# Optimization experiments

Hardware: AMD Instinct MI355X
Metric: run time of the kernel (lower is better)

Reference implementation:

```python
import jax, jax.numpy as jnp
import numpy as np

N = 131072
BETA = 1.0
E = float(np.e)
BISECT_ITERS = 60  # (v-u)/2^60 << 1e-5 threshold of FIND_MIN


def _smooth_l1(x, beta=BETA):
    d = jnp.abs(x)
    return jnp.where(d < beta, 0.5 * d * d / beta, d - 0.5 * beta)


def _safe_log(w):
    return jnp.log(jnp.maximum(w, 1e-12))


def _eps(w, wp, wh, beta=BETA):
    # epsilon(omega) = smooth_l1((omega-omega_hat)/2) + smooth_l1(log omega - log omega_p)
    return _smooth_l1((w - wh) * 0.5, beta) + _smooth_l1(_safe_log(w) - _safe_log(wp), beta)


def _eps_prime(w, wp, wh, beta=BETA):
    x = (w - wh) * 0.5
    diff = _safe_log(w) - _safe_log(wp)
    return 0.5 * jnp.clip(x / beta, -1.0, 1.0) + jnp.clip(diff / beta, -1.0, 1.0) / jnp.maximum(w, 1e-12)


def _sigma(w, wp, wh, beta=BETA):
    return w * _eps_prime(w, wp, wh, beta)


def _find_min(u, v, f):
    # Vectorized FIND_MIN bisection: fixed-trip bisection + boundary cases.
    u0, v0 = u, v

    def body(_, uv):
        uu, vv = uv
        m = (uu + vv) * 0.5
        c = f(m) >= 0
        return (jnp.where(c, uu, m), jnp.where(c, m, vv))

    uf, vf = jax.lax.fori_loop(0, BISECT_ITERS, body, (u, v))
    m = (uf + vf) * 0.5
    return jnp.where(f(u0) >= 0, u0, jnp.where(f(v0) <= 0, v0, m))


def _solve_o1(wp, wh, a1, b1, beta=BETA):
    w0 = b1 - a1
    fm_e = lambda u, v: _find_min(u, v, lambda w: _eps_prime(w, wp, wh, beta))
    fm_s = lambda u, v: _find_min(u, v, lambda w: _sigma(w, wp, wh, beta))
    branchA = jnp.maximum(w0, wh) < wp
    branchB = jnp.maximum(w0, wp) < wh
    cA = fm_e(jnp.maximum(w0, wh), wp)
    ebeta = float(np.exp(beta))
    # J1..J5 intervals from J_getter
    c2 = fm_e(jnp.maximum(w0, wp), jnp.minimum(float(np.exp(min(beta, 1.0))) * wp, wh))
    c3 = fm_e(jnp.maximum(jnp.maximum(w0, 2.0 * float(np.sqrt(beta))), jnp.maximum(wh - 2.0 * beta, ebeta * wp)), wh)
    base = jnp.maximum(w0, jnp.maximum(wh - 2.0 * beta, E * wp))
    c4 = fm_s(base, jnp.minimum(ebeta, wh))
    disc = jnp.sqrt(jnp.maximum(1.0 - 32.0 / jnp.maximum(wh * wh, 1e-12), 0.0))
    c5 = fm_s(base, jnp.minimum(jnp.minimum(ebeta * wp, wh), wh * 0.25 * (1.0 + disc)))
    c6 = fm_s(jnp.maximum(base, wh * 0.25 * (1.0 - disc)), jnp.minimum(ebeta * wp, wh))
    small = wh <= 4.0 * float(np.sqrt(2.0))
    cands = jnp.stack([w0, wh, c2, c3, c4, c5, c6], axis=-1)  # [N,7]
    evals = _eps(cands, wp[..., None], wh[..., None], beta)
    zeros = jnp.zeros_like(small)
    invalid = jnp.stack([zeros, zeros, zeros, zeros, ~small, small, small], axis=-1)
    evals = jnp.where(invalid, jnp.float32(1e30), evals)
    idx = jnp.argmin(evals, axis=-1)
    wB = jnp.take_along_axis(cands, idx[..., None], axis=-1)[..., 0]
    return jnp.where(branchA, cA, jnp.where(branchB, wB, w0))


def _solve_o2(dp, wp, a2, b2, beta=BETA):
    wh1 = 2.0 * (dp - a2)
    wh2 = 2.0 * (b2 - dp)
    trivial = wp >= jnp.maximum(wh1, wh2)
    w1 = _solve_o1(wp, wh1, a2, b2, beta)
    w2 = _solve_o1(wp, wh2, a2, b2, beta)
    pick1 = _eps(w1, wp, wh1, beta) <= _eps(w2, wp, wh2, beta)
    d = jnp.where(pick1, a2 + 0.5 * w1, b2 + 0.5 * w2)
    w = jnp.where(pick1, w1, w2)
    return jnp.where(trivial, dp, d), jnp.where(trivial, wp, w)


def _case_axis(pred, prop, cases, target, crop, axis):
    if axis == 0:
        lt, rb = cases[:, 0], cases[:, 1]
        d_id, o_id = 0, 2
    else:
        lt, rb = cases[:, 2], cases[:, 3]
        d_id, o_id = 1, 3
    pd, po = pred[:, d_id], pred[:, o_id]
    td, to = target[:, d_id], target[:, o_id]
    ca = 0.5 * (prop[:, d_id] + prop[:, o_id])
    da = prop[:, o_id] - prop[:, d_id]
    # right/bottom cut
    a1r = td - 0.5 * to
    b1r = (crop[:, axis] - ca) / da
    wr = _solve_o1(po, 2.0 * (pd - a1r), a1r, b1r)
    dr = a1r + 0.5 * wr
    # left/top cut
    a1l = -ca / da
    b1l = td + 0.5 * to
    wl = _solve_o1(po, 2.0 * (b1l - pd), a1l, b1l)
    dl = b1l - 0.5 * wl
    # both cut (source passes omega_p=pred[:,d_id] and crop[:,d_id] -- replicated)
    b2 = (crop[:, d_id] - ca) / da
    db, wb = _solve_o2(pd, pd, a1l, b2)
    none_c = (~lt) & (~rb)
    r_c = (~lt) & rb
    l_c = lt & (~rb)
    d_lab = jnp.where(none_c, td, jnp.where(r_c, dr, jnp.where(l_c, dl, db)))
    w_lab = jnp.where(none_c, to, jnp.where(r_c, wr, jnp.where(l_c, wl, wb)))
    return d_lab, w_lab


def setup_inputs() -> dict:
    key = jax.random.key(0)
    k = jax.random.split(key, 8)
    img = jax.random.normal(k[0], (1, 3, 128, 128), jnp.float32)
    pred = jax.random.normal(k[1], (N, 4), jnp.float32) * 0.3
    target = jax.random.normal(k[2], (N, 4), jnp.float32) * 0.3
    xy1 = jax.random.uniform(k[3], (N, 2), jnp.float32) * 800.0
    wh = jax.random.uniform(k[4], (N, 2), jnp.float32) * 180.0 + 20.0
    proposal_list = jnp.stack([xy1[:, 0], xy1[:, 1], xy1[:, 0] + wh[:, 0], xy1[:, 1] + wh[:, 1]], axis=1)
    crop_shapes = jax.random.uniform(k[5], (N, 4), jnp.float32) * 200.0 + 900.0
    cases = jax.random.bernoulli(k[6], 0.5, (N, 4))
    return {"img": img, "pred": pred, "target": target, "crop_shapes": crop_shapes,
            "proposal_list": proposal_list, "cases": cases, "sampling_results": 0}


def reference(img, pred, target, crop_shapes, proposal_list, cases, sampling_results):
    # target/pred dw,dh (cols 2,3) are exponentiated to widths/heights, as in forward
    predw = pred.at[:, 2:4].set(jnp.exp(pred[:, 2:4]))
    targw = target.at[:, 2:4].set(jnp.exp(target[:, 2:4]))
    d0, w0 = _case_axis(predw, proposal_list, cases, targw, crop_shapes, 0)
    d1, w1 = _case_axis(predw, proposal_list, cases, targw, crop_shapes, 1)
    # label layout [dx, dy, w, h] matching label[0..3] of the source
    return jnp.stack([d0, d1, w0, w1], axis=-1)
```

## Files before the change

kernel.cpp:

```cpp
#include <hip/hip_runtime.h>
#include <math.h>

#define BISECT_ITERS 60
#define N_ROWS 131072
#define N_PAIRS (2 * N_ROWS)
#define BLOCK 512
#define NW (BLOCK / 64)

#define E_CONST 2.71828182845904523536f
#define SMALL_THRESH 5.65685424949238019520f
#define LN2F 0.69314718055994530942f

__device__ __forceinline__ float log_cr(float wc) {
    double d = (double)wc;
    long long b = __double_as_longlong(d);
    int e = (int)((b >> 52) & 0x7FF) - 1023;
    double m = __longlong_as_double((b & 0x000FFFFFFFFFFFFFLL) |
                                    0x3FF0000000000000LL);
    if (m > 1.3333333333333333) {
        m *= 0.5;
        e += 1;
    }
    double s = (m - 1.0) / (m + 1.0);
    double s2 = s * s;
    double p = 1.0 / 17.0;
    p = fma(p, s2, 1.0 / 15.0);
    p = fma(p, s2, 1.0 / 13.0);
    p = fma(p, s2, 1.0 / 11.0);
    p = fma(p, s2, 1.0 / 9.0);
    p = fma(p, s2, 1.0 / 7.0);
    p = fma(p, s2, 1.0 / 5.0);
    p = fma(p, s2, 1.0 / 3.0);
    p = fma(p, s2, 1.0);
    double res = fma(2.0 * s, p, (double)e * 0.69314718055994530941723212145818);
    return (float)res;
}

__device__ __forceinline__ float safe_log_f(float w) {
    return log_cr(fmaxf(w, 1e-12f));
}

__device__ __forceinline__ float clip1f(float x) {
#pragma clang fp contract(off)
    return fminf(fmaxf(x, -1.0f), 1.0f);
}

__device__ __forceinline__ float sl1(float x) {
#pragma clang fp contract(off)
    float d = fabsf(x);
    return (d < 1.0f) ? (0.5f * d) * d : d - 0.5f;
}

__device__ __forceinline__ float eps_f(float w, float wh, float lwp) {
#pragma clang fp contract(off)
    return sl1((w - wh) * 0.5f) + sl1(safe_log_f(w) - lwp);
}

__device__ __forceinline__ float eps_prime_cr(float w, float wh, float lwp) {
#pragma clang fp contract(off)
    float x = (w - wh) * 0.5f;
    float diff = safe_log_f(w) - lwp;
    return 0.5f * clip1f(x) + clip1f(diff) / fmaxf(w, 1e-12f);
}

__device__ __forceinline__ float sigma_cr(float w, float wh, float lwp) {
#pragma clang fp contract(off)
    return w * eps_prime_cr(w, wh, lwp);
}

__device__ __forceinline__ float epsp_sign(float m, float wh, float lwp) {
    float wm = fmaxf(m, 1e-12f);
    float x = (m - wh) * 0.5f;
    float diff = __builtin_fmaf(LN2F, __builtin_amdgcn_logf(wm), -lwp);
    return __builtin_fmaf(0.5f * clip1f(x), wm, clip1f(diff));
}

__device__ float find_min_e(float u, float v, float wh, float lwp) {
#pragma clang fp contract(off)
    float u0 = u, v0 = v;
#pragma unroll 1
    for (int i = 0; i < BISECT_ITERS; ++i) {
        float m = (u + v) * 0.5f;
        bool frozen = (m == u) || (m == v);
        bool c = epsp_sign(m, wh, lwp) >= 0.0f;
        u = c ? u : m;
        v = c ? m : v;
        if (__all(frozen)) break;
    }
    float m = (u + v) * 0.5f;
    float r = m;
    if (eps_prime_cr(v0, wh, lwp) <= 0.0f) r = v0;
    if (eps_prime_cr(u0, wh, lwp) >= 0.0f) r = u0;
    return r;
}

struct PairP {
    float pd, po, td, to, a1r, b1r, a1l, b1l;
    int lt, rb;
};

__device__ __forceinline__ PairP load_pair(const float* __restrict__ pred,
                                           const float* __restrict__ target,
                                           const float* __restrict__ crop,
                                           const float* __restrict__ prop,
                                           const int* __restrict__ cases,
                                           int pair) {
#pragma clang fp contract(off)
    int row = pair >> 1, axis = pair & 1;
    int d_id = axis, o_id = axis + 2, r4 = row * 4;
    PairP P;
    P.pd = pred[r4 + d_id];
    P.po = (float)exp((double)pred[r4 + o_id]);
    P.td = target[r4 + d_id];
    P.to = (float)exp((double)target[r4 + o_id]);
    float p_d = prop[r4 + d_id];
    float p_o = prop[r4 + o_id];
    float ca = 0.5f * (p_d + p_o);
    float da = p_o - p_d;
    float crop_a = crop[r4 + axis];
    P.a1r = P.td - 0.5f * P.to;
    P.b1r = (crop_a - ca) / da;
    P.a1l = (-ca) / da;
    P.b1l = P.td + 0.5f * P.to;
    P.lt = cases[r4 + 2 * axis];
    P.rb = cases[r4 + 2 * axis + 1];
    return P;
}

__device__ float solve_B_large(float wp, float wh, float w0, float lwp) {
#pragma clang fp contract(off)
    float ewp = E_CONST * wp;
    float base = fmaxf(w0, fmaxf(wh - 2.0f, ewp));
    float disc = sqrtf(fmaxf(1.0f - 32.0f / fmaxf(wh * wh, 1e-12f), 0.0f));

    float u2 = fmaxf(w0, wp), v2 = fminf(ewp, wh);
    float u3 = fmaxf(fmaxf(w0, 2.0f), fmaxf(wh - 2.0f, ewp)), v3 = wh;
    float u5 = base, v5 = fminf(fminf(ewp, wh), (wh * 0.25f) * (1.0f + disc));
    float u6 = fmaxf(base, (wh * 0.25f) * (1.0f - disc)), v6 = fminf(ewp, wh);
    float u02 = u2, v02 = v2, u03 = u3, v03 = v3;
    float u05 = u5, v05 = v5, u06 = u6, v06 = v6;

#pragma unroll 1
    for (int i = 0; i < BISECT_ITERS; ++i) {
        float m2 = (u2 + v2) * 0.5f;
        float m3 = (u3 + v3) * 0.5f;
        float m5 = (u5 + v5) * 0.5f;
        float m6 = (u6 + v6) * 0.5f;
        bool fr = (m2 == u2 || m2 == v2) && (m3 == u3 || m3 == v3) &&
                  (m5 == u5 || m5 == v5) && (m6 == u6 || m6 == v6);
        bool c2 = epsp_sign(m2, wh, lwp) >= 0.0f;
        bool c3 = epsp_sign(m3, wh, lwp) >= 0.0f;
        bool c5 = (m5 * epsp_sign(m5, wh, lwp)) >= 0.0f;
        bool c6 = (m6 * epsp_sign(m6, wh, lwp)) >= 0.0f;
        u2 = c2 ? u2 : m2; v2 = c2 ? m2 : v2;
        u3 = c3 ? u3 : m3; v3 = c3 ? m3 : v3;
        u5 = c5 ? u5 : m5; v5 = c5 ? m5 : v5;
        u6 = c6 ? u6 : m6; v6 = c6 ? m6 : v6;
        if (__all(fr)) break;
    }

    float c2r = (u2 + v2) * 0.5f;
    if (eps_prime_cr(v02, wh, lwp) <= 0.0f) c2r = v02;
    if (eps_prime_cr(u02, wh, lwp) >= 0.0f) c2r = u02;
    float c3r = (u3 + v3) * 0.5f;
    if (eps_prime_cr(v03, wh, lwp) <= 0.0f) c3r = v03;
    if (eps_prime_cr(u03, wh, lwp) >= 0.0f) c3r = u03;
    float c5r = (u5 + v5) * 0.5f;
    if (sigma_cr(v05, wh, lwp) <= 0.0f) c5r = v05;
    if (sigma_cr(u05, wh, lwp) >= 0.0f) c5r = u05;
    float c6r = (u6 + v6) * 0.5f;
    if (sigma_cr(v06, wh, lwp) <= 0.0f) c6r = v06;
    if (sigma_cr(u06, wh, lwp) >= 0.0f) c6r = u06;

    float cands[7] = {w0, wh, c2r, c3r, 0.0f, c5r, c6r};
    float evals[7];
    evals[0] = eps_f(w0, wh, lwp);
    evals[1] = eps_f(wh, wh, lwp);
    evals[2] = eps_f(c2r, wh, lwp);
    evals[3] = eps_f(c3r, wh, lwp);
    evals[4] = 1e30f;
    evals[5] = eps_f(c5r, wh, lwp);
    evals[6] = eps_f(c6r, wh, lwp);

    float bestv = evals[0];
    float wB = cands[0];
#pragma unroll
    for (int j = 1; j < 7; ++j) {
        if (evals[j] < bestv) {
            bestv = evals[j];
            wB = cands[j];
        }
    }
    return wB;
}

__device__ float solve_B_small(float wp, float wh, float w0, float lwp) {
#pragma clang fp contract(off)
    float ewp = E_CONST * wp;
    float base = fmaxf(w0, fmaxf(wh - 2.0f, ewp));

    float u2 = fmaxf(w0, wp), v2 = fminf(ewp, wh);
    float u3 = fmaxf(fmaxf(w0, 2.0f), fmaxf(wh - 2.0f, ewp)), v3 = wh;
    float u4 = base, v4 = fminf(E_CONST, wh);
    float u02 = u2, v02 = v2, u03 = u3, v03 = v3, u04 = u4, v04 = v4;

#pragma unroll 1
    for (int i = 0; i < BISECT_ITERS; ++i) {
        float m2 = (u2 + v2) * 0.5f;
        float m3 = (u3 + v3) * 0.5f;
        float m4 = (u4 + v4) * 0.5f;
        bool fr = (m2 == u2 || m2 == v2) && (m3 == u3 || m3 == v3) &&
                  (m4 == u4 || m4 == v4);
        bool c2 = epsp_sign(m2, wh, lwp) >= 0.0f;
        bool c3 = epsp_sign(m3, wh, lwp) >= 0.0f;
        bool c4 = (m4 * epsp_sign(m4, wh, lwp)) >= 0.0f;
        u2 = c2 ? u2 : m2; v2 = c2 ? m2 : v2;
        u3 = c3 ? u3 : m3; v3 = c3 ? m3 : v3;
        u4 = c4 ? u4 : m4; v4 = c4 ? m4 : v4;
        if (__all(fr)) break;
    }

    float c2r = (u2 + v2) * 0.5f;
    if (eps_prime_cr(v02, wh, lwp) <= 0.0f) c2r = v02;
    if (eps_prime_cr(u02, wh, lwp) >= 0.0f) c2r = u02;
    float c3r = (u3 + v3) * 0.5f;
    if (eps_prime_cr(v03, wh, lwp) <= 0.0f) c3r = v03;
    if (eps_prime_cr(u03, wh, lwp) >= 0.0f) c3r = u03;
    float c4r = (u4 + v4) * 0.5f;
    if (sigma_cr(v04, wh, lwp) <= 0.0f) c4r = v04;
    if (sigma_cr(u04, wh, lwp) >= 0.0f) c4r = u04;

    float cands[7] = {w0, wh, c2r, c3r, c4r, 0.0f, 0.0f};
    float evals[7];
    evals[0] = eps_f(w0, wh, lwp);
    evals[1] = eps_f(wh, wh, lwp);
    evals[2] = eps_f(c2r, wh, lwp);
    evals[3] = eps_f(c3r, wh, lwp);
    evals[4] = eps_f(c4r, wh, lwp);
    evals[5] = 1e30f;
    evals[6] = 1e30f;

    float bestv = evals[0];
    float wB = cands[0];
#pragma unroll
    for (int j = 1; j < 7; ++j) {
        if (evals[j] < bestv) {
            bestv = evals[j];
            wB = cands[j];
        }
    }
    return wB;
}

__global__ __launch_bounds__(BLOCK)
void cabb_fused_kernel(const float* __restrict__ pred,
                       const float* __restrict__ target,
                       const float* __restrict__ crop,
                       const float* __restrict__ prop,
                       const int* __restrict__ cases,
                       float* __restrict__ out) {
#pragma clang fp contract(off)
    __shared__ float qb_wp[2 * BLOCK], qb_wh[2 * BLOCK], qb_w0[2 * BLOCK];
    __shared__ unsigned short qb_code[2 * BLOCK];
    __shared__ float qa_wp[BLOCK], qa_wh[BLOCK], qa_w0[BLOCK];
    __shared__ unsigned short qa_code[BLOCK];
    __shared__ float s_res[2 * BLOCK];
    __shared__ int s_cnt[NW][3];
    __shared__ int s_tot[3];

    int tid = threadIdx.x;
    int wid = tid >> 6;
    int lane = tid & 63;
    unsigned long long lower = (1ULL << lane) - 1ULL;
    int pair = blockIdx.x * BLOCK + tid;

    if (tid < 3) s_tot[tid] = 0;

    PairP P = load_pair(pred, target, crop, prop, cases, pair);

    bool need_b = P.lt && P.rb;
    bool need_l = P.lt && !P.rb;
    bool need_r = !P.lt && P.rb;

    int it_type[2] = {-1, -1};
    float it_wp[2], it_wh[2], it_w0[2];
    unsigned short it_code[2];
    int nit = 0;

    if (need_r || need_l) {
        float wp = P.po;
        float wh = need_l ? 2.0f * (P.b1l - P.pd) : 2.0f * (P.pd - P.a1r);
        float w0 = need_l ? (P.b1l - P.a1l) : (P.b1r - P.a1r);
        bool bA = fmaxf(w0, wh) < wp;
        bool bB = fmaxf(w0, wp) < wh;
        if (bA || bB) {
            it_type[0] = bA ? 2 : (wh <= SMALL_THRESH ? 1 : 0);
            it_wp[0] = wp; it_wh[0] = wh; it_w0[0] = w0;
            it_code[0] = (unsigned short)(tid * 2);
            nit = 1;
        }
    } else if (need_b) {
        float wh1 = 2.0f * (P.pd - P.a1l);
        float wh2 = 2.0f * (P.b1r - P.pd);
        bool trivial = P.pd >= fmaxf(wh1, wh2);
        if (!trivial) {
            float w0 = P.b1r - P.a1l;
            for (int s = 0; s < 2; ++s) {
                float wh = s ? wh2 : wh1;
                bool bA = fmaxf(w0, wh) < P.pd;
                bool bB = fmaxf(w0, P.pd) < wh;
                if (bA || bB) {
                    it_type[nit] = bA ? 2 : (wh <= SMALL_THRESH ? 1 : 0);
                    it_wp[nit] = P.pd; it_wh[nit] = wh; it_w0[nit] = w0;
                    it_code[nit] = (unsigned short)(tid * 2 + s);
                    ++nit;
                }
            }
        }
    }

    for (int k = 0; k < 2; ++k) {
        bool is0 = it_type[k] == 0, is1 = it_type[k] == 1, is2 = it_type[k] == 2;
        unsigned long long m0 = __ballot(is0);
        unsigned long long m1 = __ballot(is1);
        unsigned long long m2 = __ballot(is2);
        if (lane == 0) {
            s_cnt[wid][0] = __popcll(m0);
            s_cnt[wid][1] = __popcll(m1);
            s_cnt[wid][2] = __popcll(m2);
        }
        __syncthreads();
        if (it_type[k] >= 0) {
            int t = it_type[k];
            int base = s_tot[t];
            for (int w = 0; w < wid; ++w) base += s_cnt[w][t];
            unsigned long long mm = t == 0 ? m0 : (t == 1 ? m1 : m2);
            int pos = base + __popcll(mm & lower);
            if (t == 0) {
                qb_wp[pos] = it_wp[k]; qb_wh[pos] = it_wh[k];
                qb_w0[pos] = it_w0[k]; qb_code[pos] = it_code[k];
            } else if (t == 1) {
                int p2 = (2 * BLOCK - 1) - pos;
                qb_wp[p2] = it_wp[k]; qb_wh[p2] = it_wh[k];
                qb_w0[p2] = it_w0[k]; qb_code[p2] = it_code[k];
            } else {
                qa_wp[pos] = it_wp[k]; qa_wh[pos] = it_wh[k];
                qa_w0[pos] = it_w0[k]; qa_code[pos] = it_code[k];
            }
        }
        __syncthreads();
        if (tid < 3) {
            int s = 0;
            for (int w = 0; w < NW; ++w) s += s_cnt[w][tid];
            s_tot[tid] += s;
        }
        __syncthreads();
    }

    int nBl = s_tot[0], nBs = s_tot[1], nA = s_tot[2];

    for (int base = wid * 64; base < nBl; base += BLOCK) {
        int i = base + lane;
        if (i < nBl) {
            float wp = qb_wp[i], wh = qb_wh[i], w0 = qb_w0[i];
            float lwp = safe_log_f(wp);
            s_res[qb_code[i]] = solve_B_large(wp, wh, w0, lwp);
        }
    }
    for (int base = wid * 64; base < nBs; base += BLOCK) {
        int i = base + lane;
        if (i < nBs) {
            int idx = (2 * BLOCK - 1) - i;
            float wp = qb_wp[idx], wh = qb_wh[idx], w0 = qb_w0[idx];
            float lwp = safe_log_f(wp);
            s_res[qb_code[idx]] = solve_B_small(wp, wh, w0, lwp);
        }
    }
    for (int base = wid * 64; base < nA; base += BLOCK) {
        int i = base + lane;
        if (i < nA) {
            float wp = qa_wp[i], wh = qa_wh[i], w0 = qa_w0[i];
            float lwp = safe_log_f(wp);
            s_res[qa_code[i]] = find_min_e(fmaxf(w0, wh), wp, wh, lwp);
        }
    }
    __syncthreads();

    int row = pair >> 1, axis = pair & 1;
    int r4 = row * 4;
    float d_lab, w_lab;
    if (need_b) {
        float wh1 = 2.0f * (P.pd - P.a1l);
        float wh2 = 2.0f * (P.b1r - P.pd);
        bool trivial = P.pd >= fmaxf(wh1, wh2);
        if (trivial) {
            d_lab = P.pd;
            w_lab = P.pd;
        } else {
            float w0 = P.b1r - P.a1l;
            bool q1 = (fmaxf(w0, wh1) < P.pd) || (fmaxf(w0, P.pd) < wh1);
            bool q2 = (fmaxf(w0, wh2) < P.pd) || (fmaxf(w0, P.pd) < wh2);
            float s1 = q1 ? s_res[tid * 2] : w0;
            float s2 = q2 ? s_res[tid * 2 + 1] : w0;
            float lwp = safe_log_f(P.pd);
            bool pick1 = eps_f(s1, wh1, lwp) <= eps_f(s2, wh2, lwp);
            d_lab = pick1 ? (P.a1l + 0.5f * s1) : (P.b1r + 0.5f * s2);
            w_lab = pick1 ? s1 : s2;
        }
    } else if (need_l) {
        float wh = 2.0f * (P.b1l - P.pd);
        float w0 = P.b1l - P.a1l;
        bool q = (fmaxf(w0, wh) < P.po) || (fmaxf(w0, P.po) < wh);
        float s = q ? s_res[tid * 2] : w0;
        d_lab = P.b1l - 0.5f * s;
        w_lab = s;
    } else if (need_r) {
        float wh = 2.0f * (P.pd - P.a1r);
        float w0 = P.b1r - P.a1r;
        bool q = (fmaxf(w0, wh) < P.po) || (fmaxf(w0, P.po) < wh);
        float s = q ? s_res[tid * 2] : w0;
        d_lab = P.a1r + 0.5f * s;
        w_lab = s;
    } else {
        d_lab = P.td;
        w_lab = P.to;
    }

    out[r4 + axis] = d_lab;
    out[r4 + 2 + axis] = w_lab;
}

extern "C" void kernel_launch(void* const* d_in, const int* in_sizes, int n_in,
                              void* d_out, int out_size, void* d_ws, size_t ws_size,
                              hipStream_t stream) {
    const float* pred = (const float*)d_in[1];
    const float* target = (const float*)d_in[2];
    const float* crop = (const float*)d_in[3];
    const float* prop = (const float*)d_in[4];
    const int* cases = (const int*)d_in[5];
    float* out = (float*)d_out;

    cabb_fused_kernel<<<N_PAIRS / BLOCK, BLOCK, 0, stream>>>(
        pred, target, crop, prop, cases, out);
}
```

Measured before the change: 93.93 us.

## Use fast log filters with exact fallback for boundary checks and candidate selection

Endpoint sign checks, candidate-energy evaluation and the two-sided pick now use the hardware log2 approximation first. They fall back to the double-precision log only when the result lies within a tolerance band where the sign or ordering is ambiguous, which removes most of the expensive software log evaluations. The three per-queue solve loops are merged into one chunk loop that hands 64-lane chunks to wavefronts round-robin, so work is balanced across queues. The risk is that the tolerance thresholds might miss a case where the fast path disagrees with the exact path, and the fallback branches add divergence.

```diff
diff --git a/kernel.cpp b/kernel.cpp
--- a/kernel.cpp
+++ b/kernel.cpp
@@ -10,6 +10,7 @@
 #define E_CONST 2.71828182845904523536f
 #define SMALL_THRESH 5.65685424949238019520f
 #define LN2F 0.69314718055994530942f
+#define LOG1EM12 -27.63102111592854820f
 
 __device__ __forceinline__ float log_cr(float wc) {
     double d = (double)wc;
@@ -37,7 +38,8 @@
 }
 
 __device__ __forceinline__ float safe_log_f(float w) {
-    return log_cr(fmaxf(w, 1e-12f));
+    if (w <= 1e-12f) return LOG1EM12;
+    return log_cr(w);
 }
 
 __device__ __forceinline__ float clip1f(float x) {
@@ -66,6 +68,10 @@
 __device__ __forceinline__ float sigma_cr(float w, float wh, float lwp) {
 #pragma clang fp contract(off)
     return w * eps_prime_cr(w, wh, lwp);
+}
+
+__device__ __forceinline__ float nlogf(float w) {
+    return LN2F * __builtin_amdgcn_logf(fmaxf(w, 1e-12f));
 }
 
 __device__ __forceinline__ float epsp_sign(float m, float wh, float lwp) {
@@ -73,6 +79,30 @@
     float x = (m - wh) * 0.5f;
     float diff = __builtin_fmaf(LN2F, __builtin_amdgcn_logf(wm), -lwp);
     return __builtin_fmaf(0.5f * clip1f(x), wm, clip1f(diff));
+}
+
+__device__ __forceinline__ int fast_epsp_sgn(float x, float wh, float lwp) {
+    float wm = fmaxf(x, 1e-12f);
+    float F = epsp_sign(x, wh, lwp);
+    float tau = 2e-5f * (wm + 1.0f);
+    if (F > tau) return 1;
+    if (F < -tau) return -1;
+    return 0;
+}
+
+__device__ __forceinline__ int fast_sigma_sgn(float x, float wh, float lwp) {
+    float wm = fmaxf(x, 1e-12f);
+    float F = epsp_sign(x, wh, lwp);
+    float G = x * F;
+    float tau = fabsf(x) * (2e-5f * (wm + 1.0f));
+    if (G > tau) return 1;
+    if (G < -tau) return -1;
+    return 0;
+}
+
+__device__ __forceinline__ float fast_eval(float w, float wh, float lwp) {
+#pragma clang fp contract(off)
+    return sl1((w - wh) * 0.5f) + sl1(nlogf(w) - lwp);
 }
 
 __device__ float find_min_e(float u, float v, float wh, float lwp) {
@@ -92,6 +122,64 @@
     if (eps_prime_cr(v0, wh, lwp) <= 0.0f) r = v0;
     if (eps_prime_cr(u0, wh, lwp) >= 0.0f) r = u0;
     return r;
+}
+
+__device__ __forceinline__ bool ov_e_le(float x, float wh, float lwp) {
+    int s = fast_epsp_sgn(x, wh, lwp);
+    if (s < 0) return true;
+    if (s > 0) return false;
+    return eps_prime_cr(x, wh, lwp) <= 0.0f;
+}
+__device__ __forceinline__ bool ov_e_ge(float x, float wh, float lwp) {
+    int s = fast_epsp_sgn(x, wh, lwp);
+    if (s > 0) return true;
+    if (s < 0) return false;
+    return eps_prime_cr(x, wh, lwp) >= 0.0f;
+}
+__device__ __forceinline__ bool ov_s_le(float x, float wh, float lwp) {
+    int s = fast_sigma_sgn(x, wh, lwp);
+    if (s < 0) return true;
+    if (s > 0) return false;
+    return sigma_cr(x, wh, lwp) <= 0.0f;
+}
+__device__ __forceinline__ bool ov_s_ge(float x, float wh, float lwp) {
+    int s = fast_sigma_sgn(x, wh, lwp);
+    if (s > 0) return true;
+    if (s < 0) return false;
+    return sigma_cr(x, wh, lwp) >= 0.0f;
+}
+
+__device__ __forceinline__ float argmin7(const float* cands, const float* Ef,
+                                         const bool* valid, float wh, float lwp) {
+#pragma clang fp contract(off)
+    int j = 0;
+    float best = Ef[0];
+#pragma unroll
+    for (int k = 1; k < 7; ++k) {
+        if (Ef[k] < best) { best = Ef[k]; j = k; }
+    }
+    bool need_cr = false;
+#pragma unroll
+    for (int k = 0; k < 7; ++k) {
+        if (k == j) continue;
+        float dl = 2e-5f + 2e-6f * (fabsf(best) + fabsf(Ef[k]));
+        if (Ef[k] < best + dl &&
+            fabsf(cands[k] - cands[j]) > 1e-4f * (1.0f + fabsf(cands[j])))
+            need_cr = true;
+    }
+    if (need_cr) {
+        float Ec[7];
+#pragma unroll
+        for (int k = 0; k < 7; ++k)
+            Ec[k] = valid[k] ? eps_f(cands[k], wh, lwp) : 1e30f;
+        j = 0;
+        best = Ec[0];
+#pragma unroll
+        for (int k = 1; k < 7; ++k) {
+            if (Ec[k] < best) { best = Ec[k]; j = k; }
+        }
+    }
+    return cands[j];
 }
 
 struct PairP {
@@ -160,38 +248,29 @@
     }
 
     float c2r = (u2 + v2) * 0.5f;
-    if (eps_prime_cr(v02, wh, lwp) <= 0.0f) c2r = v02;
-    if (eps_prime_cr(u02, wh, lwp) >= 0.0f) c2r = u02;
+    if (ov_e_le(v02, wh, lwp)) c2r = v02;
+    if (ov_e_ge(u02, wh, lwp)) c2r = u02;
     float c3r = (u3 + v3) * 0.5f;
-    if (eps_prime_cr(v03, wh, lwp) <= 0.0f) c3r = v03;
-    if (eps_prime_cr(u03, wh, lwp) >= 0.0f) c3r = u03;
+    if (ov_e_le(v03, wh, lwp)) c3r = v03;
+    if (ov_e_ge(u03, wh, lwp)) c3r = u03;
     float c5r = (u5 + v5) * 0.5f;
-    if (sigma_cr(v05, wh, lwp) <= 0.0f) c5r = v05;
-    if (sigma_cr(u05, wh, lwp) >= 0.0f) c5r = u05;
+    if (ov_s_le(v05, wh, lwp)) c5r = v05;
+    if (ov_s_ge(u05, wh, lwp)) c5r = u05;
     float c6r = (u6 + v6) * 0.5f;
-    if (sigma_cr(v06, wh, lwp) <= 0.0f) c6r = v06;
-    if (sigma_cr(u06, wh, lwp) >= 0.0f) c6r = u06;
+    if (ov_s_le(v06, wh, lwp)) c6r = v06;
+    if (ov_s_ge(u06, wh, lwp)) c6r = u06;
 
     float cands[7] = {w0, wh, c2r, c3r, 0.0f, c5r, c6r};
-    float evals[7];
-    evals[0] = eps_f(w0, wh, lwp);
-    evals[1] = eps_f(wh, wh, lwp);
-    evals[2] = eps_f(c2r, wh, lwp);
-    evals[3] = eps_f(c3r, wh, lwp);
-    evals[4] = 1e30f;
-    evals[5] = eps_f(c5r, wh, lwp);
-    evals[6] = eps_f(c6r, wh, lwp);
-
-    float bestv = evals[0];
-    float wB = cands[0];
-#pragma unroll
-    for (int j = 1; j < 7; ++j) {
-        if (evals[j] < bestv) {
-            bestv = evals[j];
-            wB = cands[j];
-        }
-    }
-    return wB;
+    bool valid[7] = {true, true, true, true, false, true, true};
+    float Ef[7];
+    Ef[0] = fast_eval(w0, wh, lwp);
+    Ef[1] = fast_eval(wh, wh, lwp);
+    Ef[2] = fast_eval(c2r, wh, lwp);
+    Ef[3] = fast_eval(c3r, wh, lwp);
+    Ef[4] = 1e30f;
+    Ef[5] = fast_eval(c5r, wh, lwp);
+    Ef[6] = fast_eval(c6r, wh, lwp);
+    return argmin7(cands, Ef, valid, wh, lwp);
 }
 
 __device__ float solve_B_small(float wp, float wh, float w0, float lwp) {
@@ -221,35 +300,26 @@
     }
 
     float c2r = (u2 + v2) * 0.5f;
-    if (eps_prime_cr(v02, wh, lwp) <= 0.0f) c2r = v02;
-    if (eps_prime_cr(u02, wh, lwp) >= 0.0f) c2r = u02;
+    if (ov_e_le(v02, wh, lwp)) c2r = v02;
+    if (ov_e_ge(u02, wh, lwp)) c2r = u02;
     float c3r = (u3 + v3) * 0.5f;
-    if (eps_prime_cr(v03, wh, lwp) <= 0.0f) c3r = v03;
-    if (eps_prime_cr(u03, wh, lwp) >= 0.0f) c3r = u03;
+    if (ov_e_le(v03, wh, lwp)) c3r = v03;
+    if (ov_e_ge(u03, wh, lwp)) c3r = u03;
     float c4r = (u4 + v4) * 0.5f;
-    if (sigma_cr(v04, wh, lwp) <= 0.0f) c4r = v04;
-    if (sigma_cr(u04, wh, lwp) >= 0.0f) c4r = u04;
+    if (ov_s_le(v04, wh, lwp)) c4r = v04;
+    if (ov_s_ge(u04, wh, lwp)) c4r = u04;
 
     float cands[7] = {w0, wh, c2r, c3r, c4r, 0.0f, 0.0f};
-    float evals[7];
-    evals[0] = eps_f(w0, wh, lwp);
-    evals[1] = eps_f(wh, wh, lwp);
-    evals[2] = eps_f(c2r, wh, lwp);
-    evals[3] = eps_f(c3r, wh, lwp);
-    evals[4] = eps_f(c4r, wh, lwp);
-    evals[5] = 1e30f;
-    evals[6] = 1e30f;
-
-    float bestv = evals[0];
-    float wB = cands[0];
-#pragma unroll
-    for (int j = 1; j < 7; ++j) {
-        if (evals[j] < bestv) {
-            bestv = evals[j];
-            wB = cands[j];
-        }
-    }
-    return wB;
+    bool valid[7] = {true, true, true, true, true, false, false};
+    float Ef[7];
+    Ef[0] = fast_eval(w0, wh, lwp);
+    Ef[1] = fast_eval(wh, wh, lwp);
+    Ef[2] = fast_eval(c2r, wh, lwp);
+    Ef[3] = fast_eval(c3r, wh, lwp);
+    Ef[4] = fast_eval(c4r, wh, lwp);
+    Ef[5] = 1e30f;
+    Ef[6] = 1e30f;
+    return argmin7(cands, Ef, valid, wh, lwp);
 }
 
 __global__ __launch_bounds__(BLOCK)
@@ -359,29 +429,33 @@
 
     int nBl = s_tot[0], nBs = s_tot[1], nA = s_tot[2];
 
-    for (int base = wid * 64; base < nBl; base += BLOCK) {
-        int i = base + lane;
-        if (i < nBl) {
-            float wp = qb_wp[i], wh = qb_wh[i], w0 = qb_w0[i];
-            float lwp = safe_log_f(wp);
-            s_res[qb_code[i]] = solve_B_large(wp, wh, w0, lwp);
-        }
-    }
-    for (int base = wid * 64; base < nBs; base += BLOCK) {
-        int i = base + lane;
-        if (i < nBs) {
-            int idx = (2 * BLOCK - 1) - i;
-            float wp = qb_wp[idx], wh = qb_wh[idx], w0 = qb_w0[idx];
-            float lwp = safe_log_f(wp);
-            s_res[qb_code[idx]] = solve_B_small(wp, wh, w0, lwp);
-        }
-    }
-    for (int base = wid * 64; base < nA; base += BLOCK) {
-        int i = base + lane;
-        if (i < nA) {
-            float wp = qa_wp[i], wh = qa_wh[i], w0 = qa_w0[i];
-            float lwp = safe_log_f(wp);
-            s_res[qa_code[i]] = find_min_e(fmaxf(w0, wh), wp, wh, lwp);
+    int nBlC = (nBl + 63) >> 6;
+    int nBsC = (nBs + 63) >> 6;
+    int nAC = (nA + 63) >> 6;
+    int totC = nBlC + nBsC + nAC;
+    for (int c = wid; c < totC; c += NW) {
+        if (c < nBlC) {
+            int i = (c << 6) + lane;
+            if (i < nBl) {
+                float wp = qb_wp[i], wh = qb_wh[i], w0 = qb_w0[i];
+                float lwp = safe_log_f(wp);
+                s_res[qb_code[i]] = solve_B_large(wp, wh, w0, lwp);
+            }
+        } else if (c < nBlC + nBsC) {
+            int i = ((c - nBlC) << 6) + lane;
+            if (i < nBs) {
+                int idx = (2 * BLOCK - 1) - i;
+                float wp = qb_wp[idx], wh = qb_wh[idx], w0 = qb_w0[idx];
+                float lwp = safe_log_f(wp);
+                s_res[qb_code[idx]] = solve_B_small(wp, wh, w0, lwp);
+            }
+        } else {
+            int i = ((c - nBlC - nBsC) << 6) + lane;
+            if (i < nA) {
+                float wp = qa_wp[i], wh = qa_wh[i], w0 = qa_w0[i];
+                float lwp = safe_log_f(wp);
+                s_res[qa_code[i]] = find_min_e(fmaxf(w0, wh), wp, wh, lwp);
+            }
         }
     }
     __syncthreads();
@@ -402,8 +476,19 @@
             bool q2 = (fmaxf(w0, wh2) < P.pd) || (fmaxf(w0, P.pd) < wh2);
             float s1 = q1 ? s_res[tid * 2] : w0;
             float s2 = q2 ? s_res[tid * 2 + 1] : w0;
-            float lwp = safe_log_f(P.pd);
-            bool pick1 = eps_f(s1, wh1, lwp) <= eps_f(s2, wh2, lwp);
+            float lwpf = nlogf(P.pd);
+            float F1 = sl1((s1 - wh1) * 0.5f) + sl1(nlogf(s1) - lwpf);
+            float F2 = sl1((s2 - wh2) * 0.5f) + sl1(nlogf(s2) - lwpf);
+            float dl = 3e-5f + 2e-6f * (fabsf(F1) + fabsf(F2));
+            bool pick1;
+            if (F1 <= F2 - dl) {
+                pick1 = true;
+            } else if (F1 > F2 + dl) {
+                pick1 = false;
+            } else {
+                float lwp = safe_log_f(P.pd);
+                pick1 = eps_f(s1, wh1, lwp) <= eps_f(s2, wh2, lwp);
+            }
             d_lab = pick1 ? (P.a1l + 0.5f * s1) : (P.b1r + 0.5f * s2);
             w_lab = pick1 ? s1 : s2;
         }
```

Result: faster. 86.25 us (-8.2%).
